# Kernel tuning notes

Hardware: AMD Instinct MI355X
Metric: run time of the kernel (lower is better)

## Reference

```python
import jax, jax.numpy as jnp
import numpy as np

HEADS = 16
KV_HEADS = 8
HEAD_DIM = 128
ROPE_BASE = 10000.0
RMS_EPS = 1e-5


def rmsnorm(x, w, eps=RMS_EPS):
    x = jnp.clip(x.astype(jnp.float32), -100.0, 100.0)
    var = jnp.clip(jnp.mean(x * x, axis=-1, keepdims=True), eps, None)
    x = x * jax.lax.rsqrt(var + eps)
    x = jnp.clip(x, -10.0, 10.0)
    return w * x


def activation_quant(x):
    x = jnp.clip(x, -50.0, 50.0)
    max_val = jnp.clip(jnp.max(jnp.abs(x), axis=-1, keepdims=True), 0.0001, None)
    scale = 127.0 / max_val
    return jnp.clip(jnp.round(x * scale), -128.0, 127.0) / scale


def weight_quant(w):
    scale = jnp.clip(jnp.mean(jnp.abs(w)), 1e-8, None)
    e = jnp.mean(w)
    return jnp.sign(w - e) * scale


def bitlinear(x, w, norm_w):
    xn = rmsnorm(x, norm_w)
    xq = xn + jax.lax.stop_gradient(activation_quant(xn) - xn)
    wq = w + jax.lax.stop_gradient(weight_quant(w) - w)
    return xq @ wq.T


def rope_tables(seq_len, dim):
    inv_freq = 1.0 / (ROPE_BASE ** (jnp.arange(0, dim, 2, dtype=jnp.float32) / dim))
    freqs = jnp.outer(jnp.arange(seq_len, dtype=jnp.float32), inv_freq)  # [S, dim/2]
    emb = jnp.concatenate([freqs, freqs], axis=-1)  # [S, dim]
    return jnp.cos(emb), jnp.sin(emb)


def rotate_half(x):
    x1, x2 = jnp.split(x, 2, axis=-1)
    return jnp.concatenate([-x2, x1], axis=-1)


def attention_forward(hidden_states, attention_mask, wq, wk, wv, wo, nq, nk, nv, no):
    B, S, H = hidden_states.shape
    q = bitlinear(hidden_states, wq, nq)  # [B,S,nh*hd]
    k = bitlinear(hidden_states, wk, nk)  # [B,S,nkv*hd]
    v = bitlinear(hidden_states, wv, nv)

    q = q.reshape(B, S, HEADS, HEAD_DIM).transpose(0, 2, 1, 3)       # [B,nh,S,hd]
    k = k.reshape(B, S, KV_HEADS, HEAD_DIM).transpose(0, 2, 1, 3)    # [B,nkv,S,hd]
    v = v.reshape(B, S, KV_HEADS, HEAD_DIM).transpose(0, 2, 1, 3)

    cos, sin = rope_tables(S, HEAD_DIM)
    cos = cos[None, None]  # [1,1,S,hd]
    sin = sin[None, None]
    q = q * cos + rotate_half(q) * sin
    k = k * cos + rotate_half(k) * sin

    groups = HEADS // KV_HEADS
    k_exp = jnp.repeat(k, groups, axis=1)  # [B,nh,S,hd]
    v_exp = jnp.repeat(v, groups, axis=1)

    scale = 1.0 / jnp.sqrt(jnp.float32(HEAD_DIM))
    scores = jnp.einsum('bhqd,bhkd->bhqk', q, k_exp) * scale
    scores = scores + attention_mask
    attn = jax.nn.softmax(scores, axis=-1)
    out = jnp.einsum('bhqk,bhkd->bhqd', attn, v_exp)
    out = out.transpose(0, 2, 1, 3).reshape(B, S, HEADS * HEAD_DIM)
    return bitlinear(out, wo, no)


def setup_inputs() -> dict:
    key = jax.random.key(0)
    ks = jax.random.split(key, 6)
    B, S, H = 2, 2048, 2048
    KVH = KV_HEADS * HEAD_DIM
    std = 0.02 / np.sqrt(H)
    return {
        'hidden_states': jax.random.normal(ks[0], (B, S, H), jnp.float32),
        'attention_mask': jnp.zeros((1, 1, S, S), jnp.float32),
        'wq': jax.random.normal(ks[1], (H, H), jnp.float32) * std,
        'wk': jax.random.normal(ks[2], (KVH, H), jnp.float32) * std,
        'wv': jax.random.normal(ks[3], (KVH, H), jnp.float32) * std,
        'wo': jax.random.normal(ks[4], (H, H), jnp.float32) * std,
        'nq': jnp.ones((H,), jnp.float32),
        'nk': jnp.ones((H,), jnp.float32),
        'nv': jnp.ones((H,), jnp.float32),
        'no': jnp.ones((H,), jnp.float32),
    }


def reference(hidden_states, attention_mask, wq, wk, wv, wo, nq, nk, nv, no):
    return attention_forward(hidden_states, attention_mask, wq, wk, wv, wo, nq, nk, nv, no)
```

## Files before the change

### kernel.cpp

```cpp
#include <hip/hip_runtime.h>


#define DI __device__ __forceinline__

using bf16   = __bf16;
using bf16x4 = __attribute__((ext_vector_type(4))) __bf16;
using bf16x8 = __attribute__((ext_vector_type(8))) __bf16;
using f32x4  = __attribute__((ext_vector_type(4))) float;

DI void gl_lds16(void* lds, const void* g) {
  __builtin_amdgcn_global_load_lds((const __attribute__((address_space(1))) void*)g,
                                   (__attribute__((address_space(3))) void*)lds, 16, 0, 0);
}
DI float clampf(float x, float lo, float hi) { return fminf(fmaxf(x, lo), hi); }

DI float block_sum(float v, float* red, int lane, int w) {
#pragma unroll
  for (int o = 32; o > 0; o >>= 1) v += __shfl_xor(v, o, 64);
  __syncthreads();
  if (lane == 0) red[w] = v;
  __syncthreads();
  return red[0] + red[1] + red[2] + red[3];
}
DI float block_max(float v, float* red, int lane, int w) {
#pragma unroll
  for (int o = 32; o > 0; o >>= 1) v = fmaxf(v, __shfl_xor(v, o, 64));
  __syncthreads();
  if (lane == 0) red[w] = v;
  __syncthreads();
  return fmaxf(fmaxf(red[0], red[1]), fmaxf(red[2], red[3]));
}

__global__ void wstats_kernel(const float* wq, const float* wk, const float* wv,
                              const float* wo, float* stats) {
  __shared__ float red[4], red2[4];
  int t = threadIdx.x, lane = t & 63, w = t >> 6;
  int m = blockIdx.y;
  const float* src; int n4;
  if (m == 0)      { src = wq; n4 = 1048576; }
  else if (m == 1) { src = wk; n4 = 524288;  }
  else if (m == 2) { src = wv; n4 = 524288;  }
  else             { src = wo; n4 = 1048576; }
  float s = 0.f, sa = 0.f;
  for (int i = blockIdx.x * 256 + t; i < n4; i += 256 * 256) {
    float4 v = ((const float4*)src)[i];
    s  += v.x + v.y + v.z + v.w;
    sa += fabsf(v.x) + fabsf(v.y) + fabsf(v.z) + fabsf(v.w);
  }
#pragma unroll
  for (int o = 32; o > 0; o >>= 1) { s += __shfl_xor(s, o, 64); sa += __shfl_xor(sa, o, 64); }
  if (lane == 0) { red[w] = s; red2[w] = sa; }
  __syncthreads();
  if (t == 0) {
    atomicAdd(&stats[2 * m],     red[0] + red[1] + red[2] + red[3]);
    atomicAdd(&stats[2 * m + 1], red2[0] + red2[1] + red2[2] + red2[3]);
  }
}

__global__ void wsign_kernel(const float* wq, const float* wk, const float* wv, const float* wo,
                             ushort* sq, ushort* sk, ushort* sv, ushort* so,
                             const float* stats) {
  int m = blockIdx.y;
  const float* src; ushort* dst; int n4; float cinv;
  if (m == 0)      { src = wq; dst = sq; n4 = 1048576; cinv = 1.f / 4194304.f; }
  else if (m == 1) { src = wk; dst = sk; n4 = 524288;  cinv = 1.f / 2097152.f; }
  else if (m == 2) { src = wv; dst = sv; n4 = 524288;  cinv = 1.f / 2097152.f; }
  else             { src = wo; dst = so; n4 = 1048576; cinv = 1.f / 4194304.f; }
  float e = stats[2 * m] * cinv;
  for (int i = blockIdx.x * 256 + threadIdx.x; i < n4; i += 1024 * 256) {
    float4 v = ((const float4*)src)[i];
    ushort4 o;
    o.x = v.x > e ? 0x3F80 : (v.x < e ? 0xBF80 : 0);
    o.y = v.y > e ? 0x3F80 : (v.y < e ? 0xBF80 : 0);
    o.z = v.z > e ? 0x3F80 : (v.z < e ? 0xBF80 : 0);
    o.w = v.w > e ? 0x3F80 : (v.w < e ? 0xBF80 : 0);
    ((ushort4*)dst)[i] = o;
  }
}

__global__ void ropetab_kernel(float* ct, float* st) {
  int s = blockIdx.x, j = threadIdx.x;
  float invf = powf(10000.f, -(float)j * (1.f / 64.f));
  float a = (float)s * invf;
  ct[s * 64 + j] = cosf(a);
  st[s * 64 + j] = sinf(a);
}

DI void quant_one(const float* xs, const float* __restrict__ wt, bf16* __restrict__ a,
                  float* __restrict__ r, int row, int t, int lane, int w, float* red) {
  float4 w0 = ((const float4*)wt)[t * 2], w1 = ((const float4*)wt)[t * 2 + 1];
  float wv[8] = {w0.x, w0.y, w0.z, w0.w, w1.x, w1.y, w1.z, w1.w};
  float y[8]; float am = 0.f;
#pragma unroll
  for (int e = 0; e < 8; ++e) {
    y[e] = clampf(wv[e] * xs[e], -50.f, 50.f);
    am = fmaxf(am, fabsf(y[e]));
  }
  float mx = block_max(am, red, lane, w);
  float maxval = fmaxf(mx, 1e-4f);
  float sc = 127.f / maxval;
  bf16x8 q;
#pragma unroll
  for (int e = 0; e < 8; ++e) {
    float n = rintf(y[e] * sc);
    n = clampf(n, -128.f, 127.f);
    q[e] = (bf16)n;
  }
  *(bf16x8*)(a + (size_t)row * 2048 + t * 8) = q;
  if (t == 0) r[row] = maxval * (1.f / 127.f);
}

template <int NW>
__launch_bounds__(256)
__global__ void rqnorm_kernel(const float* __restrict__ x,
                              const float* __restrict__ w0, const float* __restrict__ w1,
                              const float* __restrict__ w2,
                              bf16* a0, bf16* a1, bf16* a2,
                              float* r0, float* r1, float* r2) {
  __shared__ float red[4];
  int t = threadIdx.x, lane = t & 63, w = t >> 6;
  int row = blockIdx.x;
  const float* xr = x + (size_t)row * 2048;
  float4 u0 = ((const float4*)xr)[t * 2], u1 = ((const float4*)xr)[t * 2 + 1];
  float xs[8] = {u0.x, u0.y, u0.z, u0.w, u1.x, u1.y, u1.z, u1.w};
  float ss = 0.f;
#pragma unroll
  for (int e = 0; e < 8; ++e) { xs[e] = clampf(xs[e], -100.f, 100.f); ss += xs[e] * xs[e]; }
  float tot = block_sum(ss, red, lane, w);
  float var = fmaxf(tot * (1.f / 2048.f), 1e-5f);
  float inv = 1.f / sqrtf(var + 1e-5f);
#pragma unroll
  for (int e = 0; e < 8; ++e) xs[e] = clampf(xs[e] * inv, -10.f, 10.f);
  quant_one(xs, w0, a0, r0, row, t, lane, w, red);
  if (NW > 1) quant_one(xs, w1, a1, r1, row, t, lane, w, red);
  if (NW > 2) quant_one(xs, w2, a2, r2, row, t, lane, w, red);
}

DI void mm_core(const bf16* __restrict__ Ag0, const bf16* __restrict__ Bg0,
                bf16* As, bf16* Bs, int w, int lane, f32x4 acc[2][8]) {
  int l15 = lane & 15, quad = lane >> 4;
  int srow = w * 8 + (lane >> 3);
  int sc_p = (lane & 7) * 8;
  int sc_g = ((lane & 7) ^ (lane >> 3)) * 8;
  const bf16* Ag = Ag0 + (size_t)srow * 2048 + sc_g;
  const bf16* Bg = Bg0 + (size_t)srow * 2048 + sc_g;
  bf16* Al = As + srow * 64 + sc_p;
  bf16* Bl = Bs + srow * 64 + sc_p;
  for (int kt = 0; kt < 32; ++kt) {
    size_t kb = (size_t)kt * 64;
#pragma unroll
    for (int i = 0; i < 4; ++i) {
      gl_lds16(Al + i * 32 * 64, Ag + (size_t)i * 32 * 2048 + kb);
      gl_lds16(Bl + i * 32 * 64, Bg + (size_t)i * 32 * 2048 + kb);
    }
    __syncthreads();
#pragma unroll
    for (int kc = 0; kc < 2; ++kc) {
      bf16x8 af[2], bfr[8];
#pragma unroll
      for (int mt = 0; mt < 2; ++mt)
        af[mt] = *(const bf16x8*)(As + (w * 32 + mt * 16 + l15) * 64 +
                                  (((kc * 4 + quad) ^ (l15 & 7)) * 8));
#pragma unroll
      for (int nt = 0; nt < 8; ++nt)
        bfr[nt] = *(const bf16x8*)(Bs + (nt * 16 + l15) * 64 +
                                   (((kc * 4 + quad) ^ (l15 & 7)) * 8));
#pragma unroll
      for (int mt = 0; mt < 2; ++mt)
#pragma unroll
        for (int nt = 0; nt < 8; ++nt)
          acc[mt][nt] = __builtin_amdgcn_mfma_f32_16x16x32_bf16(af[mt], bfr[nt], acc[mt][nt], 0, 0, 0);
    }
    __syncthreads();
  }
}

__launch_bounds__(256, 2)
__global__ void qkv_gemm(const bf16* __restrict__ Aq, const bf16* __restrict__ Ak,
                         const bf16* __restrict__ Av, const bf16* __restrict__ Ball,
                         const float* __restrict__ rq, const float* __restrict__ rk,
                         const float* __restrict__ rv, const float* __restrict__ stats,
                         bf16* __restrict__ qr, bf16* __restrict__ kr,
                         float* __restrict__ vlin,
                         const float* __restrict__ ct, const float* __restrict__ st) {
  __shared__ bf16 As[128 * 64];
  __shared__ bf16 Bs[128 * 64];
  int t = threadIdx.x, w = t >> 6, lane = t & 63;
  int l15 = lane & 15, quad = lane >> 4;
  int x = blockIdx.x, m0 = blockIdx.y * 128;
  const bf16* A; const float* rs; float sw; int brow0;
  if (x < 16)      { A = Aq; rs = rq; sw = stats[1] * (1.f / 4194304.f); brow0 = x * 128; }
  else if (x < 24) { A = Ak; rs = rk; sw = stats[3] * (1.f / 2097152.f); brow0 = 2048 + (x - 16) * 128; }
  else             { A = Av; rs = rv; sw = stats[5] * (1.f / 2097152.f); brow0 = 3072 + (x - 24) * 128; }
  sw = fmaxf(sw, 1e-8f);
  f32x4 acc[2][8] = {};
  mm_core(A + (size_t)m0 * 2048, Ball + (size_t)brow0 * 2048, As, Bs, w, lane, acc);

  if (x < 24) {
    bf16* outb = (x < 16) ? qr : kr;
    int h = (x < 16) ? x : x - 16;
    int nh = (x < 16) ? 16 : 8;
#pragma unroll
    for (int mt = 0; mt < 2; ++mt)
#pragma unroll
      for (int r = 0; r < 4; ++r) {
        int row = m0 + w * 32 + mt * 16 + quad * 4 + r;
        float rsc = rs[row] * sw;
        int s = row & 2047, b = row >> 11;
        size_t base = ((size_t)(b * nh + h) * 2048 + s) * 128;
#pragma unroll
        for (int nt = 0; nt < 4; ++nt) {
          int d = nt * 16 + l15;
          float x1 = acc[mt][nt][r] * rsc;
          float x2 = acc[mt][nt + 4][r] * rsc;
          float c = ct[s * 64 + d], sn = st[s * 64 + d];
          outb[base + d]      = (bf16)(x1 * c - x2 * sn);
          outb[base + d + 64] = (bf16)(x2 * c + x1 * sn);
        }
      }
  } else {
    int n0 = (x - 24) * 128;
#pragma unroll
    for (int mt = 0; mt < 2; ++mt)
#pragma unroll
      for (int r = 0; r < 4; ++r) {
        int row = m0 + w * 32 + mt * 16 + quad * 4 + r;
        float rsc = rs[row] * sw;
#pragma unroll
        for (int nt = 0; nt < 8; ++nt)
          vlin[(size_t)row * 1024 + n0 + nt * 16 + l15] = acc[mt][nt][r] * rsc;
      }
  }
}

__launch_bounds__(256, 2)
__global__ void gemm_o(const bf16* __restrict__ A, const bf16* __restrict__ Bw,
                       const float* __restrict__ rs, const float* __restrict__ stats,
                       float* __restrict__ out) {
  __shared__ bf16 As[128 * 64];
  __shared__ bf16 Bs[128 * 64];
  int t = threadIdx.x, w = t >> 6, lane = t & 63;
  int l15 = lane & 15, quad = lane >> 4;
  int m0 = blockIdx.y * 128, n0 = blockIdx.x * 128;
  f32x4 acc[2][8] = {};
  mm_core(A + (size_t)m0 * 2048, Bw + (size_t)n0 * 2048, As, Bs, w, lane, acc);
  float sw = fmaxf(stats[7] * (1.f / 4194304.f), 1e-8f);
#pragma unroll
  for (int mt = 0; mt < 2; ++mt)
#pragma unroll
    for (int r = 0; r < 4; ++r) {
      int row = m0 + w * 32 + mt * 16 + quad * 4 + r;
      float rsc = rs[row] * sw;
#pragma unroll
      for (int nt = 0; nt < 8; ++nt)
        out[(size_t)row * 2048 + n0 + nt * 16 + l15] = acc[mt][nt][r] * rsc;
    }
}

__global__ void vtrans_kernel(const float* __restrict__ v_lin, bf16* __restrict__ v_t) {
  __shared__ float tile[64][65];
  int t = threadIdx.x, c = t & 63, rq = t >> 6;
  int ct0 = blockIdx.x * 64, tt0 = blockIdx.y * 64;
#pragma unroll
  for (int i = 0; i < 16; ++i) {
    int r = rq * 16 + i;
    tile[r][c] = v_lin[(size_t)(tt0 + r) * 1024 + ct0 + c];
  }
  __syncthreads();
  int token = tt0 + c;
  int b = token >> 11, s = token & 2047;
#pragma unroll
  for (int i = 0; i < 16; ++i) {
    int cg = ct0 + rq * 16 + i;
    int kvh = cg >> 7, d = cg & 127;
    v_t[((size_t)(b * 8 + kvh) * 128 + d) * 2048 + s] = (bf16)tile[c][rq * 16 + i];
  }
}

__launch_bounds__(256, 2)
__global__ void attn_kernel(const bf16* __restrict__ Q, const bf16* __restrict__ Kc,
                            const bf16* __restrict__ Vt, const float* __restrict__ mask,
                            float* __restrict__ Oout) {
  constexpr float scale = 0.08838834764831845f;
  __shared__ bf16 Ks[2][64 * 128];
  __shared__ bf16 Vs[2][128 * 64];
  __shared__ bf16 Ps[128 * 64];
  int t = threadIdx.x, w = t >> 6, lane = t & 63;
  int l15 = lane & 15, quad = lane >> 4;
  int bh = blockIdx.y, b = bh >> 4, h = bh & 15, kvh = h >> 1;
  int q0 = blockIdx.x * 128;
  const bf16* Qb = Q + (size_t)(b * 16 + h) * 2048 * 128;
  const bf16* Kb = Kc + (size_t)(b * 8 + kvh) * 2048 * 128;
  const bf16* Vb = Vt + (size_t)(b * 8 + kvh) * 128 * 2048;

  int qloc = w * 32 + l15;
  int qg = q0 + qloc;

  bf16x8 qf[2][4];
#pragma unroll
  for (int qt = 0; qt < 2; ++qt)
#pragma unroll
    for (int kc = 0; kc < 4; ++kc)
      qf[qt][kc] = *(const bf16x8*)(Qb + (size_t)(qg + qt * 16) * 128 + kc * 32 + quad * 8);

  f32x4 Oa[8][2] = {};
  float mrow[2] = {-1e30f, -1e30f}, lrow[2] = {0.f, 0.f};

  int krow = w * 4 + quad;
  int kcol_p = l15 * 8;
  int kcol_g = (l15 ^ krow) * 8;
  int vrow = w * 8 + (lane >> 3);
  int vc_p = (lane & 7) * 8;
  int vc_g = ((lane & 7) ^ (lane >> 3)) * 8;

  auto stage = [&](int buf, int kt) {
    int kk0 = kt * 64;
#pragma unroll
    for (int i = 0; i < 4; ++i)
      gl_lds16(&Ks[buf][(i * 16 + krow) * 128 + kcol_p],
               Kb + (size_t)(kk0 + i * 16 + krow) * 128 + kcol_g);
#pragma unroll
    for (int i = 0; i < 4; ++i)
      gl_lds16(&Vs[buf][(i * 32 + vrow) * 64 + vc_p],
               Vb + (size_t)(i * 32 + vrow) * 2048 + kk0 + vc_g);
  };

  stage(0, 0);

  f32x4 mv[2][4], mvn[2][4];
#pragma unroll
  for (int qt = 0; qt < 2; ++qt)
#pragma unroll
    for (int k2 = 0; k2 < 4; ++k2)
      mv[qt][k2] = *(const f32x4*)(mask + (size_t)(qg + qt * 16) * 2048 + k2 * 16 + quad * 4);

  for (int kt = 0; kt < 32; ++kt) {
    int cur = kt & 1;
    __syncthreads();
    if (kt < 31) stage(cur ^ 1, kt + 1);

    f32x4 Sacc[4][2] = {};
#pragma unroll
    for (int kc = 0; kc < 4; ++kc) {
      bf16x8 kf[4];
#pragma unroll
      for (int k2 = 0; k2 < 4; ++k2)
        kf[k2] = *(const bf16x8*)(&Ks[cur][(k2 * 16 + l15) * 128 + (((kc * 4 + quad) ^ l15) * 8)]);
#pragma unroll
      for (int k2 = 0; k2 < 4; ++k2)
#pragma unroll
        for (int qt = 0; qt < 2; ++qt)
          Sacc[k2][qt] = __builtin_amdgcn_mfma_f32_16x16x32_bf16(kf[k2], qf[qt][kc], Sacc[k2][qt], 0, 0, 0);
    }

#pragma unroll
    for (int qt = 0; qt < 2; ++qt) {
#pragma unroll
      for (int k2 = 0; k2 < 4; ++k2)
#pragma unroll
        for (int r = 0; r < 4; ++r)
          Sacc[k2][qt][r] = Sacc[k2][qt][r] * scale + mv[qt][k2][r];
      f32x4 vm = Sacc[0][qt];
#pragma unroll
      for (int k2 = 1; k2 < 4; ++k2)
#pragma unroll
        for (int r = 0; r < 4; ++r) vm[r] = fmaxf(vm[r], Sacc[k2][qt][r]);
      float mx = fmaxf(fmaxf(vm[0], vm[1]), fmaxf(vm[2], vm[3]));
      mx = fmaxf(mx, __shfl_xor(mx, 16, 64));
      mx = fmaxf(mx, __shfl_xor(mx, 32, 64));
      float mnew = fmaxf(mrow[qt], mx);
      float alpha = __expf(mrow[qt] - mnew);
      mrow[qt] = mnew;
      f32x4 vs = {0.f, 0.f, 0.f, 0.f};
#pragma unroll
      for (int k2 = 0; k2 < 4; ++k2)
#pragma unroll
        for (int r = 0; r < 4; ++r) {
          float p = __expf(Sacc[k2][qt][r] - mnew);
          Sacc[k2][qt][r] = p;
          vs[r] += p;
        }
      float rsum = (vs[0] + vs[1]) + (vs[2] + vs[3]);
      rsum += __shfl_xor(rsum, 16, 64);
      rsum += __shfl_xor(rsum, 32, 64);
      lrow[qt] = lrow[qt] * alpha + rsum;
#pragma unroll
      for (int dt = 0; dt < 8; ++dt) Oa[dt][qt] *= alpha;
      int qr = qloc + qt * 16;
#pragma unroll
      for (int k2 = 0; k2 < 4; ++k2) {
        bf16x4 pk;
#pragma unroll
        for (int r = 0; r < 4; ++r) pk[r] = (bf16)Sacc[k2][qt][r];
        int c = k2 * 2 + (quad >> 1);
        *(bf16x4*)(&Ps[qr * 64 + ((c ^ (qr & 7)) * 8) + (quad & 1) * 4]) = pk;
      }
    }

    if (kt < 31) {
      int kk1 = (kt + 1) * 64;
#pragma unroll
      for (int qt = 0; qt < 2; ++qt)
#pragma unroll
        for (int k2 = 0; k2 < 4; ++k2)
          mvn[qt][k2] = *(const f32x4*)(mask + (size_t)(qg + qt * 16) * 2048 + kk1 + k2 * 16 + quad * 4);
    }

#pragma unroll
    for (int kc = 0; kc < 2; ++kc) {
      bf16x8 pf[2];
#pragma unroll
      for (int qt = 0; qt < 2; ++qt)
        pf[qt] = *(const bf16x8*)(&Ps[(qloc + qt * 16) * 64 + (((kc * 4 + quad) ^ (l15 & 7)) * 8)]);
#pragma unroll
      for (int dt = 0; dt < 8; ++dt) {
        bf16x8 vf = *(const bf16x8*)(&Vs[cur][(dt * 16 + l15) * 64 +
                                              (((kc * 4 + quad) ^ (l15 & 7)) * 8)]);
#pragma unroll
        for (int qt = 0; qt < 2; ++qt)
          Oa[dt][qt] = __builtin_amdgcn_mfma_f32_16x16x32_bf16(vf, pf[qt], Oa[dt][qt], 0, 0, 0);
      }
    }

#pragma unroll
    for (int qt = 0; qt < 2; ++qt)
#pragma unroll
      for (int k2 = 0; k2 < 4; ++k2) mv[qt][k2] = mvn[qt][k2];
  }

#pragma unroll
  for (int qt = 0; qt < 2; ++qt) {
    float inv = 1.f / lrow[qt];
    int token = b * 2048 + qg + qt * 16;
#pragma unroll
    for (int dt = 0; dt < 8; ++dt) {
      f32x4 o = Oa[dt][qt] * inv;
      *(f32x4*)(Oout + (size_t)token * 2048 + h * 128 + dt * 16 + quad * 4) = o;
    }
  }
}

extern "C" void kernel_launch(void* const* d_in, const int* in_sizes, int n_in,
                              void* d_out, int out_size, void* d_ws, size_t ws_size,
                              hipStream_t stream) {
  const float* hidden = (const float*)d_in[0];
  const float* mask   = (const float*)d_in[1];
  const float* wq = (const float*)d_in[2];
  const float* wk = (const float*)d_in[3];
  const float* wv = (const float*)d_in[4];
  const float* wo = (const float*)d_in[5];
  const float* nq = (const float*)d_in[6];
  const float* nk = (const float*)d_in[7];
  const float* nv = (const float*)d_in[8];
  const float* no = (const float*)d_in[9];
  float* out = (float*)d_out;
  char* ws = (char*)d_ws;

  constexpr size_t O_STATS = 0;
  constexpr size_t O_CT    = 256;
  constexpr size_t O_ST    = O_CT + 524288;
  constexpr size_t O_SQ    = O_ST + 524288;
  constexpr size_t O_SK    = O_SQ + 8388608;
  constexpr size_t O_SV    = O_SK + 4194304;
  constexpr size_t O_SO    = O_SV + 4194304;
  constexpr size_t O_RSQ   = O_SO + 8388608;
  constexpr size_t O_RSK   = O_RSQ + 16384;
  constexpr size_t O_RSV   = O_RSK + 16384;
  constexpr size_t O_RSO   = O_RSV + 16384;
  constexpr size_t O_AQQ   = O_RSO + 16384;
  constexpr size_t O_AQK   = O_AQQ + 16777216;
  constexpr size_t O_AQV   = O_AQK + 16777216;
  constexpr size_t O_QR    = O_AQV + 16777216;
  constexpr size_t O_KR    = O_QR + 16777216;
  constexpr size_t O_VT    = O_KR + 8388608;
  constexpr size_t O_VLIN2 = O_VT + 8388608;
  constexpr size_t O_ATTN  = O_AQQ;
  constexpr size_t O_AQO   = O_AQV;

  float* stats = (float*)(ws + O_STATS);
  float* ct = (float*)(ws + O_CT);
  float* st = (float*)(ws + O_ST);

  (void)hipMemsetAsync(ws + O_STATS, 0, 256, stream);

  wstats_kernel<<<dim3(256, 4), 256, 0, stream>>>(wq, wk, wv, wo, stats);
  wsign_kernel<<<dim3(1024, 4), 256, 0, stream>>>(wq, wk, wv, wo,
      (ushort*)(ws + O_SQ), (ushort*)(ws + O_SK), (ushort*)(ws + O_SV), (ushort*)(ws + O_SO), stats);
  ropetab_kernel<<<dim3(2048), 64, 0, stream>>>(ct, st);

  rqnorm_kernel<3><<<dim3(4096), 256, 0, stream>>>(hidden, nq, nk, nv,
      (bf16*)(ws + O_AQQ), (bf16*)(ws + O_AQK), (bf16*)(ws + O_AQV),
      (float*)(ws + O_RSQ), (float*)(ws + O_RSK), (float*)(ws + O_RSV));

  qkv_gemm<<<dim3(32, 32), 256, 0, stream>>>(
      (const bf16*)(ws + O_AQQ), (const bf16*)(ws + O_AQK), (const bf16*)(ws + O_AQV),
      (const bf16*)(ws + O_SQ),
      (const float*)(ws + O_RSQ), (const float*)(ws + O_RSK), (const float*)(ws + O_RSV),
      stats, (bf16*)(ws + O_QR), (bf16*)(ws + O_KR), (float*)(ws + O_VLIN2), ct, st);

  vtrans_kernel<<<dim3(16, 64), 256, 0, stream>>>((const float*)(ws + O_VLIN2), (bf16*)(ws + O_VT));

  attn_kernel<<<dim3(16, 32), 256, 0, stream>>>(
      (const bf16*)(ws + O_QR), (const bf16*)(ws + O_KR), (const bf16*)(ws + O_VT),
      mask, (float*)(ws + O_ATTN));

  rqnorm_kernel<1><<<dim3(4096), 256, 0, stream>>>((const float*)(ws + O_ATTN), no, no, no,
      (bf16*)(ws + O_AQO), (bf16*)(ws + O_AQO), (bf16*)(ws + O_AQO),
      (float*)(ws + O_RSO), (float*)(ws + O_RSO), (float*)(ws + O_RSO));

  gemm_o<<<dim3(16, 32), 256, 0, stream>>>(
      (const bf16*)(ws + O_AQO), (const bf16*)(ws + O_SO), (float*)(ws + O_RSO), stats, out);

  (void)in_sizes; (void)n_in; (void)out_size; (void)ws_size;
}
```

Baseline: 443.6 us.

## Use 8 waves per attention block, fold scale into Q, add lazy rescale

```diff
diff --git a/kernel.cpp b/kernel.cpp
--- a/kernel.cpp
+++ b/kernel.cpp
@@ -197,6 +197,8 @@
   mm_core(A + (size_t)m0 * 2048, Ball + (size_t)brow0 * 2048, As, Bs, w, lane, acc);
 
   if (x < 24) {
+    constexpr float QROPE = 0.08838834764831845f * 1.4426950408889634f;
+    float qmul = (x < 16) ? QROPE : 1.f;
     bf16* outb = (x < 16) ? qr : kr;
     int h = (x < 16) ? x : x - 16;
     int nh = (x < 16) ? 16 : 8;
@@ -205,7 +207,7 @@
 #pragma unroll
       for (int r = 0; r < 4; ++r) {
         int row = m0 + w * 32 + mt * 16 + quad * 4 + r;
-        float rsc = rs[row] * sw;
+        float rsc = rs[row] * sw * qmul;
         int s = row & 2047, b = row >> 11;
         size_t base = ((size_t)(b * nh + h) * 2048 + s) * 128;
 #pragma unroll
@@ -277,11 +279,12 @@
   }
 }
 
-__launch_bounds__(256, 2)
+__launch_bounds__(512, 4)
 __global__ void attn_kernel(const bf16* __restrict__ Q, const bf16* __restrict__ Kc,
                             const bf16* __restrict__ Vt, const float* __restrict__ mask,
                             float* __restrict__ Oout) {
-  constexpr float scale = 0.08838834764831845f;
+  constexpr float L2E  = 1.4426950408889634f;
+  constexpr float DTHR = 8.f * L2E;
   __shared__ bf16 Ks[2][64 * 128];
   __shared__ bf16 Vs[2][128 * 64];
   __shared__ bf16 Ps[128 * 64];
@@ -293,53 +296,49 @@
   const bf16* Kb = Kc + (size_t)(b * 8 + kvh) * 2048 * 128;
   const bf16* Vb = Vt + (size_t)(b * 8 + kvh) * 128 * 2048;
 
-  int qloc = w * 32 + l15;
+  int qloc = w * 16 + l15;
   int qg = q0 + qloc;
 
-  bf16x8 qf[2][4];
-#pragma unroll
-  for (int qt = 0; qt < 2; ++qt)
-#pragma unroll
-    for (int kc = 0; kc < 4; ++kc)
-      qf[qt][kc] = *(const bf16x8*)(Qb + (size_t)(qg + qt * 16) * 128 + kc * 32 + quad * 8);
-
-  f32x4 Oa[8][2] = {};
-  float mrow[2] = {-1e30f, -1e30f}, lrow[2] = {0.f, 0.f};
-
-  int krow = w * 4 + quad;
-  int kcol_p = l15 * 8;
-  int kcol_g = (l15 ^ krow) * 8;
-  int vrow = w * 8 + (lane >> 3);
-  int vc_p = (lane & 7) * 8;
-  int vc_g = ((lane & 7) ^ (lane >> 3)) * 8;
+  bf16x8 qf[4];
+#pragma unroll
+  for (int kc = 0; kc < 4; ++kc)
+    qf[kc] = *(const bf16x8*)(Qb + (size_t)qg * 128 + kc * 32 + quad * 8);
+
+  f32x4 Oa[8] = {};
+  float mrow = -1e30f, lrow = 0.f;
 
   auto stage = [&](int buf, int kt) {
     int kk0 = kt * 64;
 #pragma unroll
-    for (int i = 0; i < 4; ++i)
-      gl_lds16(&Ks[buf][(i * 16 + krow) * 128 + kcol_p],
-               Kb + (size_t)(kk0 + i * 16 + krow) * 128 + kcol_g);
-#pragma unroll
-    for (int i = 0; i < 4; ++i)
-      gl_lds16(&Vs[buf][(i * 32 + vrow) * 64 + vc_p],
-               Vb + (size_t)(i * 32 + vrow) * 2048 + kk0 + vc_g);
+    for (int i = 0; i < 2; ++i) {
+      int c = t + i * 512;
+      int kr = c >> 4, c16 = c & 15;
+      gl_lds16(&Ks[buf][c * 8],
+               Kb + (size_t)(kk0 + kr) * 128 + ((c16 ^ (kr & 15)) * 8));
+    }
+#pragma unroll
+    for (int i = 0; i < 2; ++i) {
+      int c = t + i * 512;
+      int vr = c >> 3, c8 = c & 7;
+      gl_lds16(&Vs[buf][c * 8],
+               Vb + (size_t)vr * 2048 + kk0 + ((c8 ^ (vr & 7)) * 8));
+    }
   };
 
   stage(0, 0);
 
-  f32x4 mv[2][4], mvn[2][4];
-#pragma unroll
-  for (int qt = 0; qt < 2; ++qt)
-#pragma unroll
-    for (int k2 = 0; k2 < 4; ++k2)
-      mv[qt][k2] = *(const f32x4*)(mask + (size_t)(qg + qt * 16) * 2048 + k2 * 16 + quad * 4);
+  f32x4 mv[4];
+#pragma unroll
+  for (int k2 = 0; k2 < 4; ++k2)
+    mv[k2] = *(const f32x4*)(mask + (size_t)qg * 2048 + k2 * 16 + quad * 4);
 
   for (int kt = 0; kt < 32; ++kt) {
     int cur = kt & 1;
     __syncthreads();
     if (kt < 31) stage(cur ^ 1, kt + 1);
 
-    f32x4 Sacc[4][2] = {};
+    f32x4 Sacc[4] = {};
+    __builtin_amdgcn_s_setprio(1);
 #pragma unroll
     for (int kc = 0; kc < 4; ++kc) {
       bf16x8 kf[4];
@@ -348,95 +347,75 @@
         kf[k2] = *(const bf16x8*)(&Ks[cur][(k2 * 16 + l15) * 128 + (((kc * 4 + quad) ^ l15) * 8)]);
 #pragma unroll
       for (int k2 = 0; k2 < 4; ++k2)
-#pragma unroll
-        for (int qt = 0; qt < 2; ++qt)
-          Sacc[k2][qt] = __builtin_amdgcn_mfma_f32_16x16x32_bf16(kf[k2], qf[qt][kc], Sacc[k2][qt], 0, 0, 0);
-    }
-
-#pragma unroll
-    for (int qt = 0; qt < 2; ++qt) {
-#pragma unroll
-      for (int k2 = 0; k2 < 4; ++k2)
-#pragma unroll
-        for (int r = 0; r < 4; ++r)
-          Sacc[k2][qt][r] = Sacc[k2][qt][r] * scale + mv[qt][k2][r];
-      f32x4 vm = Sacc[0][qt];
-#pragma unroll
-      for (int k2 = 1; k2 < 4; ++k2)
-#pragma unroll
-        for (int r = 0; r < 4; ++r) vm[r] = fmaxf(vm[r], Sacc[k2][qt][r]);
-      float mx = fmaxf(fmaxf(vm[0], vm[1]), fmaxf(vm[2], vm[3]));
-      mx = fmaxf(mx, __shfl_xor(mx, 16, 64));
-      mx = fmaxf(mx, __shfl_xor(mx, 32, 64));
-      float mnew = fmaxf(mrow[qt], mx);
-      float alpha = __expf(mrow[qt] - mnew);
-      mrow[qt] = mnew;
-      f32x4 vs = {0.f, 0.f, 0.f, 0.f};
-#pragma unroll
-      for (int k2 = 0; k2 < 4; ++k2)
-#pragma unroll
-        for (int r = 0; r < 4; ++r) {
-          float p = __expf(Sacc[k2][qt][r] - mnew);
-          Sacc[k2][qt][r] = p;
-          vs[r] += p;
-        }
-      float rsum = (vs[0] + vs[1]) + (vs[2] + vs[3]);
-      rsum += __shfl_xor(rsum, 16, 64);
-      rsum += __shfl_xor(rsum, 32, 64);
-      lrow[qt] = lrow[qt] * alpha + rsum;
-#pragma unroll
-      for (int dt = 0; dt < 8; ++dt) Oa[dt][qt] *= alpha;
-      int qr = qloc + qt * 16;
-#pragma unroll
-      for (int k2 = 0; k2 < 4; ++k2) {
-        bf16x4 pk;
-#pragma unroll
-        for (int r = 0; r < 4; ++r) pk[r] = (bf16)Sacc[k2][qt][r];
-        int c = k2 * 2 + (quad >> 1);
-        *(bf16x4*)(&Ps[qr * 64 + ((c ^ (qr & 7)) * 8) + (quad & 1) * 4]) = pk;
+        Sacc[k2] = __builtin_amdgcn_mfma_f32_16x16x32_bf16(kf[k2], qf[kc], Sacc[k2], 0, 0, 0);
+    }
+    __builtin_amdgcn_s_setprio(0);
+
+#pragma unroll
+    for (int k2 = 0; k2 < 4; ++k2)
+#pragma unroll
+      for (int r = 0; r < 4; ++r)
+        Sacc[k2][r] = fmaf(mv[k2][r], L2E, Sacc[k2][r]);
+    f32x4 vm;
+#pragma unroll
+    for (int r = 0; r < 4; ++r)
+      vm[r] = fmaxf(fmaxf(Sacc[0][r], Sacc[1][r]), fmaxf(Sacc[2][r], Sacc[3][r]));
+    float mx = fmaxf(fmaxf(vm[0], vm[1]), fmaxf(vm[2], vm[3]));
+    mx = fmaxf(mx, __shfl_xor(mx, 16, 64));
+    mx = fmaxf(mx, __shfl_xor(mx, 32, 64));
+    if (!__all(mx <= mrow + DTHR)) {
+      float mnew = fmaxf(mrow, mx);
+      float alpha = exp2f(mrow - mnew);
+      mrow = mnew;
+      lrow *= alpha;
+#pragma unroll
+      for (int dt = 0; dt < 8; ++dt) Oa[dt] *= alpha;
+    }
+    f32x4 vs = {0.f, 0.f, 0.f, 0.f};
+#pragma unroll
+    for (int k2 = 0; k2 < 4; ++k2) {
+      bf16x4 pk;
+#pragma unroll
+      for (int r = 0; r < 4; ++r) {
+        float p = exp2f(Sacc[k2][r] - mrow);
+        vs[r] += p;
+        pk[r] = (bf16)p;
       }
-    }
+      int c = k2 * 2 + (quad >> 1);
+      *(bf16x4*)(&Ps[qloc * 64 + ((c ^ (qloc & 7)) * 8) + (quad & 1) * 4]) = pk;
+    }
+    float rsum = (vs[0] + vs[1]) + (vs[2] + vs[3]);
+    rsum += __shfl_xor(rsum, 16, 64);
+    rsum += __shfl_xor(rsum, 32, 64);
+    lrow += rsum;
 
     if (kt < 31) {
       int kk1 = (kt + 1) * 64;
 #pragma unroll
-      for (int qt = 0; qt < 2; ++qt)
-#pragma unroll
-        for (int k2 = 0; k2 < 4; ++k2)
-          mvn[qt][k2] = *(const f32x4*)(mask + (size_t)(qg + qt * 16) * 2048 + kk1 + k2 * 16 + quad * 4);
-    }
-
+      for (int k2 = 0; k2 < 4; ++k2)
+        mv[k2] = *(const f32x4*)(mask + (size_t)qg * 2048 + kk1 + k2 * 16 + quad * 4);
+    }
+
+    __builtin_amdgcn_s_setprio(1);
 #pragma unroll
     for (int kc = 0; kc < 2; ++kc) {
-      bf16x8 pf[2];
-#pragma unroll
-      for (int qt = 0; qt < 2; ++qt)
-        pf[qt] = *(const bf16x8*)(&Ps[(qloc + qt * 16) * 64 + (((kc * 4 + quad) ^ (l15 & 7)) * 8)]);
+      bf16x8 pf = *(const bf16x8*)(&Ps[qloc * 64 + (((kc * 4 + quad) ^ (l15 & 7)) * 8)]);
 #pragma unroll
       for (int dt = 0; dt < 8; ++dt) {
         bf16x8 vf = *(const bf16x8*)(&Vs[cur][(dt * 16 + l15) * 64 +
                                               (((kc * 4 + quad) ^ (l15 & 7)) * 8)]);
-#pragma unroll
-        for (int qt = 0; qt < 2; ++qt)
-          Oa[dt][qt] = __builtin_amdgcn_mfma_f32_16x16x32_bf16(vf, pf[qt], Oa[dt][qt], 0, 0, 0);
+        Oa[dt] = __builtin_amdgcn_mfma_f32_16x16x32_bf16(vf, pf, Oa[dt], 0, 0, 0);
       }
     }
-
-#pragma unroll
-    for (int qt = 0; qt < 2; ++qt)
-#pragma unroll
-      for (int k2 = 0; k2 < 4; ++k2) mv[qt][k2] = mvn[qt][k2];
-  }
-
-#pragma unroll
-  for (int qt = 0; qt < 2; ++qt) {
-    float inv = 1.f / lrow[qt];
-    int token = b * 2048 + qg + qt * 16;
-#pragma unroll
-    for (int dt = 0; dt < 8; ++dt) {
-      f32x4 o = Oa[dt][qt] * inv;
-      *(f32x4*)(Oout + (size_t)token * 2048 + h * 128 + dt * 16 + quad * 4) = o;
-    }
+    __builtin_amdgcn_s_setprio(0);
+  }
+
+  float inv = 1.f / lrow;
+  int token = b * 2048 + qg;
+#pragma unroll
+  for (int dt = 0; dt < 8; ++dt) {
+    f32x4 o = Oa[dt] * inv;
+    *(f32x4*)(Oout + (size_t)token * 2048 + h * 128 + dt * 16 + quad * 4) = o;
   }
 }
 
@@ -500,7 +479,7 @@
 
   vtrans_kernel<<<dim3(16, 64), 256, 0, stream>>>((const float*)(ws + O_VLIN2), (bf16*)(ws + O_VT));
 
-  attn_kernel<<<dim3(16, 32), 256, 0, stream>>>(
+  attn_kernel<<<dim3(16, 32), 512, 0, stream>>>(
       (const bf16*)(ws + O_QR), (const bf16*)(ws + O_KR), (const bf16*)(ws + O_VT),
       mask, (float*)(ws + O_ATTN));
 
```

Result: faster. 424.2 us (-4.4%).
